# Kernel tuning notes

Measured on AMD Instinct MI355X. Metric: run time of the kernel, lower is better.

## Reference

```python
import jax, jax.numpy as jnp
import numpy as np

N, E, D, H, L = 50000, 800000, 64, 4, 2
DH = D // H


def layer_norm(h, g, b, eps=1e-5):
    mu = h.mean(-1, keepdims=True)
    var = ((h - mu) ** 2).mean(-1, keepdims=True)
    return (h - mu) / jnp.sqrt(var + eps) * g + b


def setup_inputs() -> dict:
    key = jax.random.key(0)
    ks = jax.random.split(key, 16)
    s = 1.0 / np.sqrt(D)
    inp = {
        "x": jax.random.normal(ks[0], (N, D), jnp.float32),
        "edge_attr": jax.random.normal(ks[1], (E, D), jnp.float32),
        "edge_index": jax.random.randint(ks[2], (2, E), 0, N, jnp.int64),
        "WQ": jax.random.normal(ks[3], (L, D, D), jnp.float32) * s,
        "WK": jax.random.normal(ks[4], (L, D, D), jnp.float32) * s,
        "WE": jax.random.normal(ks[5], (L, D, D), jnp.float32) * s,
        "WV": jax.random.normal(ks[6], (L, D, D), jnp.float32) * s,
        "WO": jax.random.normal(ks[7], (L, D, D), jnp.float32) * s,
        "bO": jnp.zeros((L, D), jnp.float32),
        "ln1_g": jnp.ones((L, D), jnp.float32),
        "ln1_b": jnp.zeros((L, D), jnp.float32),
        "W1": jax.random.normal(ks[8], (L, D, 2 * D), jnp.float32) * s,
        "b1": jnp.zeros((L, 2 * D), jnp.float32),
        "W2": jax.random.normal(ks[9], (L, 2 * D, D), jnp.float32) * (1.0 / np.sqrt(2 * D)),
        "b2": jnp.zeros((L, D), jnp.float32),
        "ln2_g": jnp.ones((L, D), jnp.float32),
        "ln2_b": jnp.zeros((L, D), jnp.float32),
    }
    return inp


def exphormer_layer(h, edge_attr, src, dst, p):
    (wq, wk, we, wv, wo, bo, g1, be1, w1, b1, w2, b2, g2, be2) = p
    n = h.shape[0]
    Qh = (h @ wq).reshape(n, H, DH)
    Kh = (h @ wk).reshape(n, H, DH)
    Vh = (h @ wv).reshape(n, H, DH)
    Eh = (edge_attr @ we).reshape(-1, H, DH)
    # per-edge score: sum over head_dim of K[src]*Q[dst]*E / sqrt(DH)
    s = jnp.sum(Kh[src] * Qh[dst] * Eh, axis=-1, keepdims=True) / np.sqrt(DH)
    score = jnp.exp(jnp.clip(s, -5.0, 5.0))  # [E, H, 1]
    msg = Vh[src] * score                     # [E, H, DH]
    wV = jax.ops.segment_sum(msg, dst, num_segments=n)    # [N, H, DH]
    Z = jax.ops.segment_sum(score, dst, num_segments=n)   # [N, H, 1]
    h_attn = (wV / (Z + 1e-6)).reshape(n, D)
    h1 = layer_norm(h + (h_attn @ wo + bo), g1, be1)
    ffn = jax.nn.relu(h1 @ w1 + b1) @ w2 + b2
    return layer_norm(h1 + ffn, g2, be2)


def reference(x, edge_attr, edge_index, WQ, WK, WE, WV, WO, bO, ln1_g, ln1_b,
              W1, b1, W2, b2, ln2_g, ln2_b):
    src = edge_index[0]
    dst = edge_index[1]
    h = x
    for l in range(L):
        p = (WQ[l], WK[l], WE[l], WV[l], WO[l], bO[l], ln1_g[l], ln1_b[l],
             W1[l], b1[l], W2[l], b2[l], ln2_g[l], ln2_b[l])
        h = exphormer_layer(h, edge_attr, src, dst, p)
    return h
```

## Files before the change

kernel.cpp:

```cpp
#include <hip/hip_runtime.h>

#define NN 50000
#define NE 800000
#define D  64
#define NL 2
#define NB 196

typedef __bf16 bf16x8 __attribute__((ext_vector_type(8)));
typedef float  floatx4 __attribute__((ext_vector_type(4)));

static __device__ __forceinline__ float bf2f(unsigned short u) {
    return __uint_as_float(((unsigned)u) << 16);
}
static __device__ __forceinline__ unsigned short f2bf(float x) {
    unsigned u = __float_as_uint(x);
    u += 0x7fff + ((u >> 16) & 1);
    return (unsigned short)(u >> 16);
}


__global__ void k_deg(const int* __restrict__ ei, int* __restrict__ deg) {
    int e = blockIdx.x * 256 + threadIdx.x;
    if (e < NE) atomicAdd(&deg[ei[NE + e]], 1);
}

__global__ __launch_bounds__(256) void k_scan1(const int* __restrict__ deg,
                                               int* __restrict__ psum) {
    __shared__ int red[4];
    int i = blockIdx.x * 256 + threadIdx.x;
    int v = (i < NN) ? deg[i] : 0;
#pragma unroll
    for (int m = 1; m < 64; m <<= 1) v += __shfl_xor(v, m, 64);
    if ((threadIdx.x & 63) == 0) red[threadIdx.x >> 6] = v;
    __syncthreads();
    if (threadIdx.x == 0) psum[blockIdx.x] = red[0] + red[1] + red[2] + red[3];
}

__global__ void k_scan2(int* __restrict__ psum) {
    __shared__ int buf[256];
    int t = threadIdx.x;
    int v = (t < NB) ? psum[t] : 0;
    buf[t] = v;
    __syncthreads();
    for (int o = 1; o < 256; o <<= 1) {
        int x = (t >= o) ? buf[t - o] : 0;
        __syncthreads();
        buf[t] += x;
        __syncthreads();
    }
    if (t < NB) psum[t] = buf[t] - v;
}

__global__ __launch_bounds__(256) void k_scan3(const int* __restrict__ deg,
                                               const int* __restrict__ psum,
                                               int* __restrict__ row_off,
                                               int* __restrict__ cursor) {
    __shared__ int buf[256];
    int t = threadIdx.x;
    int i = blockIdx.x * 256 + t;
    int v = (i < NN) ? deg[i] : 0;
    buf[t] = v;
    __syncthreads();
    for (int o = 1; o < 256; o <<= 1) {
        int x = (t >= o) ? buf[t - o] : 0;
        __syncthreads();
        buf[t] += x;
        __syncthreads();
    }
    if (i < NN) {
        int inc = buf[t] + psum[blockIdx.x];
        row_off[i + 1] = inc;
        cursor[i] = inc - v;
        if (i == 0) row_off[0] = 0;
    }
}

__global__ void k_scatter(const int* __restrict__ ei, int* __restrict__ cursor,
                          int* __restrict__ csr_src, int* __restrict__ eperm) {
    int e = blockIdx.x * 256 + threadIdx.x;
    if (e < NE) {
        int dst = ei[NE + e];
        int pos = atomicAdd(&cursor[dst], 1);
        csr_src[pos] = ei[e];
        eperm[e] = pos;
    }
}

__global__ __launch_bounds__(256) void k_prep(
        const float* __restrict__ WQ, const float* __restrict__ WK,
        const float* __restrict__ WV, const float* __restrict__ WE,
        const float* __restrict__ WO, const float* __restrict__ W1,
        const float* __restrict__ W2,
        unsigned short* __restrict__ wqT, unsigned short* __restrict__ wkT,
        unsigned short* __restrict__ wvT, unsigned short* __restrict__ weT,
        unsigned short* __restrict__ woT, unsigned short* __restrict__ w1T,
        unsigned short* __restrict__ w2T) {
    int idx = blockIdx.x * 256 + threadIdx.x;
    if (idx >= 2 * 36864) return;
    int l = idx / 36864;
    int r = idx % 36864;
    if (r < 20480) {
        int which = r >> 12, rr = r & 4095;
        int m = rr >> 6, k = rr & 63;
        const float* src = (which == 0 ? WQ : which == 1 ? WK : which == 2 ? WV :
                            which == 3 ? WE : WO);
        unsigned short* dst = (which == 0 ? wqT : which == 1 ? wkT : which == 2 ? wvT :
                               which == 3 ? weT : woT);
        dst[l * 4096 + rr] = f2bf(src[l * 4096 + k * 64 + m]);
    } else if (r < 28672) {
        int r2 = r - 20480;
        int m = r2 >> 6, k = r2 & 63;
        w1T[l * 8192 + r2] = f2bf(W1[l * 8192 + k * 128 + m]);
    } else {
        int r3 = r - 28672;
        int m = r3 >> 7, k = r3 & 127;
        w2T[l * 8192 + r3] = f2bf(W2[l * 8192 + k * 64 + m]);
    }
}


__global__ __launch_bounds__(256) void k_qkv_mfma(const float* __restrict__ h,
        const unsigned short* __restrict__ wqT, const unsigned short* __restrict__ wkT,
        const unsigned short* __restrict__ wvT,
        float* __restrict__ Qh, unsigned short* __restrict__ Kb,
        unsigned short* __restrict__ Vb) {
    __shared__ unsigned short st[4][16 * 72];
    const int lane = threadIdx.x & 63;
    const int w    = threadIdx.x >> 6;
    const int ml   = lane & 15;
    const int quad = lane >> 4;

    bf16x8 aq[2][4], ak[2][4], av[2][4];
#pragma unroll
    for (int kt = 0; kt < 2; kt++)
#pragma unroll
        for (int mt = 0; mt < 4; mt++) {
            int o = (mt*16 + ml)*64 + kt*32 + quad*8;
            aq[kt][mt] = *(const bf16x8*)&wqT[o];
            ak[kt][mt] = *(const bf16x8*)&wkT[o];
            av[kt][mt] = *(const bf16x8*)&wvT[o];
        }

    const int wave = blockIdx.x * 4 + w;
    const int nw   = gridDim.x * 4;
    for (int tile = wave; tile < NN / 16; tile += nw) {
        const int e0 = tile * 16;
        const float4* ar = (const float4*)(h + (size_t)(e0 + ml) * D);
        bf16x8 b[2];
#pragma unroll
        for (int kt = 0; kt < 2; kt++) {
            float4 f0 = ar[kt*8 + quad*2 + 0];
            float4 f1 = ar[kt*8 + quad*2 + 1];
            b[kt][0] = (__bf16)f0.x; b[kt][1] = (__bf16)f0.y;
            b[kt][2] = (__bf16)f0.z; b[kt][3] = (__bf16)f0.w;
            b[kt][4] = (__bf16)f1.x; b[kt][5] = (__bf16)f1.y;
            b[kt][6] = (__bf16)f1.z; b[kt][7] = (__bf16)f1.w;
        }
        floatx4 accq[4] = {}, acck[4] = {}, accv[4] = {};
#pragma unroll
        for (int kt = 0; kt < 2; kt++)
#pragma unroll
            for (int mt = 0; mt < 4; mt++) {
                accq[mt] = __builtin_amdgcn_mfma_f32_16x16x32_bf16(aq[kt][mt], b[kt], accq[mt], 0, 0, 0);
                acck[mt] = __builtin_amdgcn_mfma_f32_16x16x32_bf16(ak[kt][mt], b[kt], acck[mt], 0, 0, 0);
                accv[mt] = __builtin_amdgcn_mfma_f32_16x16x32_bf16(av[kt][mt], b[kt], accv[mt], 0, 0, 0);
            }
#pragma unroll
        for (int mt = 0; mt < 4; mt++)
            *(float4*)(Qh + (size_t)(e0 + ml) * D + mt*16 + quad*4) =
                make_float4(accq[mt][0], accq[mt][1], accq[mt][2], accq[mt][3]);
        const int el = lane >> 2, c = lane & 3;
#pragma unroll
        for (int mt = 0; mt < 4; mt++)
            *(ushort4*)&st[w][ml*72 + mt*16 + quad*4] =
                make_ushort4(f2bf(acck[mt][0]), f2bf(acck[mt][1]),
                             f2bf(acck[mt][2]), f2bf(acck[mt][3]));
        {
            uint4 r0 = *(const uint4*)&st[w][el*72 + c*16 + 0];
            uint4 r1 = *(const uint4*)&st[w][el*72 + c*16 + 8];
            uint4* gp = (uint4*)(Kb + (size_t)(e0 + el) * D + c*16);
            gp[0] = r0; gp[1] = r1;
        }
#pragma unroll
        for (int mt = 0; mt < 4; mt++)
            *(ushort4*)&st[w][ml*72 + mt*16 + quad*4] =
                make_ushort4(f2bf(accv[mt][0]), f2bf(accv[mt][1]),
                             f2bf(accv[mt][2]), f2bf(accv[mt][3]));
        {
            uint4 r0 = *(const uint4*)&st[w][el*72 + c*16 + 0];
            uint4 r1 = *(const uint4*)&st[w][el*72 + c*16 + 8];
            uint4* gp = (uint4*)(Vb + (size_t)(e0 + el) * D + c*16);
            gp[0] = r0; gp[1] = r1;
        }
    }
}

__global__ __launch_bounds__(256) void k_eh_mfma(const float* __restrict__ ea,
        const unsigned short* __restrict__ weT, const int* __restrict__ eperm,
        unsigned short* __restrict__ Eh) {
    __shared__ unsigned short st[4][16 * 72];
    const int lane = threadIdx.x & 63;
    const int w    = threadIdx.x >> 6;
    const int ml   = lane & 15;
    const int quad = lane >> 4;

    bf16x8 afr[2][2][4];
#pragma unroll
    for (int l = 0; l < 2; l++)
#pragma unroll
        for (int kt = 0; kt < 2; kt++)
#pragma unroll
            for (int mt = 0; mt < 4; mt++)
                afr[l][kt][mt] = *(const bf16x8*)&weT[l*4096 + (mt*16 + ml)*64 + kt*32 + quad*8];

    const int wave = blockIdx.x * 4 + w;
    const int nw   = gridDim.x * 4;
    const int el = lane >> 2, c = lane & 3;
    for (int tile = wave; tile < NE / 16; tile += nw) {
        const int e0 = tile * 16;
        const float4* ar = (const float4*)(ea + (size_t)(e0 + ml) * D);
        bf16x8 b[2];
#pragma unroll
        for (int kt = 0; kt < 2; kt++) {
            float4 f0 = ar[kt*8 + quad*2 + 0];
            float4 f1 = ar[kt*8 + quad*2 + 1];
            b[kt][0] = (__bf16)f0.x; b[kt][1] = (__bf16)f0.y;
            b[kt][2] = (__bf16)f0.z; b[kt][3] = (__bf16)f0.w;
            b[kt][4] = (__bf16)f1.x; b[kt][5] = (__bf16)f1.y;
            b[kt][6] = (__bf16)f1.z; b[kt][7] = (__bf16)f1.w;
        }
        int pos = eperm[e0 + el];
#pragma unroll
        for (int l = 0; l < 2; l++) {
            floatx4 acc[4] = {};
#pragma unroll
            for (int kt = 0; kt < 2; kt++)
#pragma unroll
                for (int mt = 0; mt < 4; mt++)
                    acc[mt] = __builtin_amdgcn_mfma_f32_16x16x32_bf16(afr[l][kt][mt], b[kt], acc[mt], 0, 0, 0);
#pragma unroll
            for (int mt = 0; mt < 4; mt++)
                *(ushort4*)&st[w][ml*72 + mt*16 + quad*4] =
                    make_ushort4(f2bf(acc[mt][0]), f2bf(acc[mt][1]),
                                 f2bf(acc[mt][2]), f2bf(acc[mt][3]));
            uint4 r0 = *(const uint4*)&st[w][el*72 + c*16 + 0];
            uint4 r1 = *(const uint4*)&st[w][el*72 + c*16 + 8];
            uint4* gp = (uint4*)(Eh + (size_t)l * NE * D + (size_t)pos * D + c*16);
            gp[0] = r0;
            gp[1] = r1;
        }
    }
}

__global__ __launch_bounds__(256) void k_agg(const float* __restrict__ Qh,
        const unsigned short* __restrict__ Kb, const unsigned short* __restrict__ Vb,
        const unsigned short* __restrict__ Eh,
        const int* __restrict__ row_off, const int* __restrict__ csr_src,
        float* __restrict__ h_attn) {
    const int node = blockIdx.x * 4 + (threadIdx.x >> 6);
    if (node >= NN) return;
    const int lane  = threadIdx.x & 63;
    const int eslot = lane >> 4;
    const int ml    = lane & 15;
    const int beg = row_off[node], end = row_off[node + 1];
    const float4 q = ((const float4*)(Qh + (size_t)node * D))[ml];
    float4 acc = make_float4(0.f, 0.f, 0.f, 0.f);
    float z = 0.f;

    for (int cbeg = beg; cbeg < end; cbeg += 64) {
        const int cnt = min(64, end - cbeg);
        int myidx = cbeg + lane;
        int mysrc = (myidx < end) ? csr_src[myidx] : 0;

        for (int base = 0; base < cnt; base += 16) {
            int  jj[4];
            int  s[4];
            bool act[4];
#pragma unroll
            for (int u = 0; u < 4; u++) {
                int j = base + eslot + 4 * u;
                act[u] = j < cnt;
                jj[u]  = act[u] ? j : 0;
                s[u]   = __shfl(mysrc, jj[u], 64);
            }
            ushort4 kb[4], eb[4], vb[4];
#pragma unroll
            for (int u = 0; u < 4; u++) {
                kb[u] = *(const ushort4*)(Kb + (size_t)s[u] * D + ml * 4);
                eb[u] = *(const ushort4*)(Eh + (size_t)(cbeg + jj[u]) * D + ml * 4);
                vb[u] = *(const ushort4*)(Vb + (size_t)s[u] * D + ml * 4);
            }
#pragma unroll
            for (int u = 0; u < 4; u++) {
                float part = bf2f(kb[u].x) * q.x * bf2f(eb[u].x)
                           + bf2f(kb[u].y) * q.y * bf2f(eb[u].y)
                           + bf2f(kb[u].z) * q.z * bf2f(eb[u].z)
                           + bf2f(kb[u].w) * q.w * bf2f(eb[u].w);
                part += __shfl_xor(part, 1, 64);
                part += __shfl_xor(part, 2, 64);
                float sc = act[u] ? __expf(fminf(5.f, fmaxf(-5.f, part * 0.25f))) : 0.f;
                acc.x += sc * bf2f(vb[u].x);
                acc.y += sc * bf2f(vb[u].y);
                acc.z += sc * bf2f(vb[u].z);
                acc.w += sc * bf2f(vb[u].w);
                z += sc;
            }
        }
    }
#pragma unroll
    for (int m = 16; m <= 32; m <<= 1) {
        acc.x += __shfl_xor(acc.x, m, 64);
        acc.y += __shfl_xor(acc.y, m, 64);
        acc.z += __shfl_xor(acc.z, m, 64);
        acc.w += __shfl_xor(acc.w, m, 64);
        z     += __shfl_xor(z, m, 64);
    }
    if (eslot == 0) {
        float inv = 1.f / (z + 1e-6f);
        ((float4*)(h_attn + (size_t)node * D))[ml] =
            make_float4(acc.x * inv, acc.y * inv, acc.z * inv, acc.w * inv);
    }
}

__global__ __launch_bounds__(512) void k_post_mfma(const float* __restrict__ h_in,
        const float* __restrict__ h_attn,
        const unsigned short* __restrict__ woT_g,
        const unsigned short* __restrict__ w1T_g,
        const unsigned short* __restrict__ w2T_g,
        const float* __restrict__ bo,
        const float* __restrict__ g1, const float* __restrict__ be1,
        const float* __restrict__ b1, const float* __restrict__ b2,
        const float* __restrict__ g2, const float* __restrict__ be2,
        float* __restrict__ h_out) {
    __shared__ unsigned short woT_s[64 * 72];
    __shared__ unsigned short w1T_s[128 * 72];
    __shared__ unsigned short w2T_s[64 * 136];
    __shared__ unsigned short stg[8][16 * 136];

    const int t = threadIdx.x;
    {
        const uint4* s0 = (const uint4*)woT_g;
        { int i = t; if (i < 512) { int row = i >> 3, c = i & 7;
              *(uint4*)&woT_s[row*72 + c*8] = s0[i]; } }
        const uint4* s1 = (const uint4*)w1T_g;
        for (int i = t; i < 1024; i += 512) {
            int row = i >> 3, c = i & 7;
            *(uint4*)&w1T_s[row*72 + c*8] = s1[i];
        }
        const uint4* s2 = (const uint4*)w2T_g;
        for (int i = t; i < 1024; i += 512) {
            int row = i >> 4, c = i & 15;
            *(uint4*)&w2T_s[row*136 + c*8] = s2[i];
        }
    }
    __syncthreads();

    const int w = t >> 6, lane = t & 63;
    const int ml = lane & 15, quad = lane >> 4;
    const int tile = blockIdx.x * 8 + w;
    if (tile >= NN / 16) return;
    const int e0 = tile * 16;
    unsigned short* st = stg[w];

    const float4* ap = (const float4*)(h_attn + (size_t)(e0 + ml) * D);
    floatx4 acc1[4] = {};
#pragma unroll
    for (int kt = 0; kt < 2; kt++) {
        float4 f0 = ap[kt*8 + quad*2 + 0];
        float4 f1 = ap[kt*8 + quad*2 + 1];
        bf16x8 b;
        b[0] = (__bf16)f0.x; b[1] = (__bf16)f0.y; b[2] = (__bf16)f0.z; b[3] = (__bf16)f0.w;
        b[4] = (__bf16)f1.x; b[5] = (__bf16)f1.y; b[6] = (__bf16)f1.z; b[7] = (__bf16)f1.w;
#pragma unroll
        for (int mt = 0; mt < 4; mt++) {
            bf16x8 a = *(const bf16x8*)&woT_s[(mt*16 + ml)*72 + kt*32 + quad*8];
            acc1[mt] = __builtin_amdgcn_mfma_f32_16x16x32_bf16(a, b, acc1[mt], 0, 0, 0);
        }
    }
    const float4* hp  = (const float4*)(h_in + (size_t)(e0 + ml) * D);
    const float4* bo4 = (const float4*)bo;
    floatx4 tt[4];
#pragma unroll
    for (int mt = 0; mt < 4; mt++) {
        float4 hh = hp[mt*4 + quad];
        float4 bb = bo4[mt*4 + quad];
        tt[mt][0] = acc1[mt][0] + hh.x + bb.x;
        tt[mt][1] = acc1[mt][1] + hh.y + bb.y;
        tt[mt][2] = acc1[mt][2] + hh.z + bb.z;
        tt[mt][3] = acc1[mt][3] + hh.w + bb.w;
    }
    float s = 0.f;
#pragma unroll
    for (int mt = 0; mt < 4; mt++) s += tt[mt][0] + tt[mt][1] + tt[mt][2] + tt[mt][3];
    s += __shfl_xor(s, 16, 64); s += __shfl_xor(s, 32, 64);
    float mu = s * (1.f / 64.f);
    float v = 0.f;
#pragma unroll
    for (int mt = 0; mt < 4; mt++)
#pragma unroll
        for (int r = 0; r < 4; r++) { float c = tt[mt][r] - mu; v += c * c; }
    v += __shfl_xor(v, 16, 64); v += __shfl_xor(v, 32, 64);
    float rstd = rsqrtf(v * (1.f / 64.f) + 1e-5f);
    const float4* g1v  = (const float4*)g1;
    const float4* be1v = (const float4*)be1;
    floatx4 h1[4];
#pragma unroll
    for (int mt = 0; mt < 4; mt++) {
        float4 gg = g1v[mt*4 + quad];
        float4 bb = be1v[mt*4 + quad];
        h1[mt][0] = (tt[mt][0] - mu) * rstd * gg.x + bb.x;
        h1[mt][1] = (tt[mt][1] - mu) * rstd * gg.y + bb.y;
        h1[mt][2] = (tt[mt][2] - mu) * rstd * gg.z + bb.z;
        h1[mt][3] = (tt[mt][3] - mu) * rstd * gg.w + bb.w;
        *(ushort4*)&st[ml*136 + mt*16 + quad*4] =
            make_ushort4(f2bf(h1[mt][0]), f2bf(h1[mt][1]), f2bf(h1[mt][2]), f2bf(h1[mt][3]));
    }

    bf16x8 bh[2];
#pragma unroll
    for (int kt = 0; kt < 2; kt++)
        bh[kt] = *(const bf16x8*)&st[ml*136 + kt*32 + quad*8];
    floatx4 acc2[8] = {};
#pragma unroll
    for (int kt = 0; kt < 2; kt++)
#pragma unroll
        for (int mt = 0; mt < 8; mt++) {
            bf16x8 a = *(const bf16x8*)&w1T_s[(mt*16 + ml)*72 + kt*32 + quad*8];
            acc2[mt] = __builtin_amdgcn_mfma_f32_16x16x32_bf16(a, bh[kt], acc2[mt], 0, 0, 0);
        }
    const float4* b1v = (const float4*)b1;
#pragma unroll
    for (int mt = 0; mt < 8; mt++) {
        float4 bb = b1v[mt*4 + quad];
        float y0 = fmaxf(acc2[mt][0] + bb.x, 0.f);
        float y1 = fmaxf(acc2[mt][1] + bb.y, 0.f);
        float y2 = fmaxf(acc2[mt][2] + bb.z, 0.f);
        float y3 = fmaxf(acc2[mt][3] + bb.w, 0.f);
        *(ushort4*)&st[ml*136 + mt*16 + quad*4] =
            make_ushort4(f2bf(y0), f2bf(y1), f2bf(y2), f2bf(y3));
    }

    floatx4 acc3[4] = {};
#pragma unroll
    for (int kt = 0; kt < 4; kt++) {
        bf16x8 b = *(const bf16x8*)&st[ml*136 + kt*32 + quad*8];
#pragma unroll
        for (int mt = 0; mt < 4; mt++) {
            bf16x8 a = *(const bf16x8*)&w2T_s[(mt*16 + ml)*136 + kt*32 + quad*8];
            acc3[mt] = __builtin_amdgcn_mfma_f32_16x16x32_bf16(a, b, acc3[mt], 0, 0, 0);
        }
    }
    const float4* b2v = (const float4*)b2;
#pragma unroll
    for (int mt = 0; mt < 4; mt++) {
        float4 bb = b2v[mt*4 + quad];
        tt[mt][0] = acc3[mt][0] + bb.x + h1[mt][0];
        tt[mt][1] = acc3[mt][1] + bb.y + h1[mt][1];
        tt[mt][2] = acc3[mt][2] + bb.z + h1[mt][2];
        tt[mt][3] = acc3[mt][3] + bb.w + h1[mt][3];
    }
    s = 0.f;
#pragma unroll
    for (int mt = 0; mt < 4; mt++) s += tt[mt][0] + tt[mt][1] + tt[mt][2] + tt[mt][3];
    s += __shfl_xor(s, 16, 64); s += __shfl_xor(s, 32, 64);
    mu = s * (1.f / 64.f);
    v = 0.f;
#pragma unroll
    for (int mt = 0; mt < 4; mt++)
#pragma unroll
        for (int r = 0; r < 4; r++) { float c = tt[mt][r] - mu; v += c * c; }
    v += __shfl_xor(v, 16, 64); v += __shfl_xor(v, 32, 64);
    rstd = rsqrtf(v * (1.f / 64.f) + 1e-5f);
    const float4* g2v  = (const float4*)g2;
    const float4* be2v = (const float4*)be2;
    float4* outp = (float4*)(h_out + (size_t)(e0 + ml) * D);
#pragma unroll
    for (int mt = 0; mt < 4; mt++) {
        float4 gg = g2v[mt*4 + quad];
        float4 bb = be2v[mt*4 + quad];
        float4 o;
        o.x = (tt[mt][0] - mu) * rstd * gg.x + bb.x;
        o.y = (tt[mt][1] - mu) * rstd * gg.y + bb.y;
        o.z = (tt[mt][2] - mu) * rstd * gg.z + bb.z;
        o.w = (tt[mt][3] - mu) * rstd * gg.w + bb.w;
        outp[mt*4 + quad] = o;
    }
}


extern "C" void kernel_launch(void* const* d_in, const int* in_sizes, int n_in,
                              void* d_out, int out_size, void* d_ws, size_t ws_size,
                              hipStream_t stream) {
    const float* x   = (const float*)d_in[0];
    const float* ea  = (const float*)d_in[1];
    const int*   ei  = (const int*)d_in[2];
    const float* WQ  = (const float*)d_in[3];
    const float* WK  = (const float*)d_in[4];
    const float* WE  = (const float*)d_in[5];
    const float* WV  = (const float*)d_in[6];
    const float* WO  = (const float*)d_in[7];
    const float* bO  = (const float*)d_in[8];
    const float* g1  = (const float*)d_in[9];
    const float* be1 = (const float*)d_in[10];
    const float* W1  = (const float*)d_in[11];
    const float* b1  = (const float*)d_in[12];
    const float* W2  = (const float*)d_in[13];
    const float* b2  = (const float*)d_in[14];
    const float* g2  = (const float*)d_in[15];
    const float* be2 = (const float*)d_in[16];
    float* out = (float*)d_out;

    char* wsb = (char*)d_ws;
    size_t off = 0;
    auto alloc = [&](size_t bytes) {
        void* p = wsb + off;
        off += (bytes + 255) & ~(size_t)255;
        return p;
    };
    float* Qh            = (float*)alloc((size_t)NN * D * 4);
    unsigned short* Kb   = (unsigned short*)alloc((size_t)NN * D * 2);
    unsigned short* Vb   = (unsigned short*)alloc((size_t)NN * D * 2);
    float* hbuf          = (float*)alloc((size_t)NN * D * 4);
    float* hattn         = (float*)alloc((size_t)NN * D * 4);
    unsigned short* Eh   = (unsigned short*)alloc((size_t)NL * NE * D * 2);
    int* row_off         = (int*)alloc((size_t)(NN + 1) * 4);
    int* cursor          = (int*)alloc((size_t)NN * 4);
    int* deg             = (int*)alloc((size_t)NN * 4);
    int* psum            = (int*)alloc((size_t)256 * 4);
    int* csr_src         = (int*)alloc((size_t)NE * 4);
    int* eperm           = (int*)alloc((size_t)NE * 4);
    unsigned short* wqT  = (unsigned short*)alloc((size_t)2 * 4096 * 2);
    unsigned short* wkT  = (unsigned short*)alloc((size_t)2 * 4096 * 2);
    unsigned short* wvT  = (unsigned short*)alloc((size_t)2 * 4096 * 2);
    unsigned short* weT  = (unsigned short*)alloc((size_t)2 * 4096 * 2);
    unsigned short* woT  = (unsigned short*)alloc((size_t)2 * 4096 * 2);
    unsigned short* w1T  = (unsigned short*)alloc((size_t)2 * 8192 * 2);
    unsigned short* w2T  = (unsigned short*)alloc((size_t)2 * 8192 * 2);

    hipMemsetAsync(deg, 0, (size_t)NN * 4, stream);
    k_deg<<<(NE + 255) / 256, 256, 0, stream>>>(ei, deg);
    k_scan1<<<NB, 256, 0, stream>>>(deg, psum);
    k_scan2<<<1, 256, 0, stream>>>(psum);
    k_scan3<<<NB, 256, 0, stream>>>(deg, psum, row_off, cursor);
    k_scatter<<<(NE + 255) / 256, 256, 0, stream>>>(ei, cursor, csr_src, eperm);
    k_prep<<<(2 * 36864 + 255) / 256, 256, 0, stream>>>(WQ, WK, WV, WE, WO, W1, W2,
            wqT, wkT, wvT, weT, woT, w1T, w2T);
    k_eh_mfma<<<1024, 256, 0, stream>>>(ea, weT, eperm, Eh);

    for (int l = 0; l < NL; l++) {
        const float* hcur = (l == 0) ? x : hbuf;
        float* hnxt = (l == NL - 1) ? out : hbuf;
        k_qkv_mfma<<<782, 256, 0, stream>>>(hcur, wqT + l * 4096, wkT + l * 4096,
                                            wvT + l * 4096, Qh, Kb, Vb);
        k_agg<<<(NN + 3) / 4, 256, 0, stream>>>(Qh, Kb, Vb, Eh + (size_t)l * NE * D,
                                                row_off, csr_src, hattn);
        k_post_mfma<<<(NN / 16 + 7) / 8, 512, 0, stream>>>(hcur, hattn,
                woT + l * 4096, w1T + l * 8192, w2T + l * 8192,
                bO + l * 64, g1 + l * 64, be1 + l * 64,
                b1 + l * 128, b2 + l * 64,
                g2 + l * 64, be2 + l * 64, hnxt);
    }
}
```

Measured before the change: 611.3 us.

## Fuse layer-0 edge scores into Eh projection, split score computation from aggregation

The layer-0 edge-attribute projection now computes the per-edge attention scores directly from MFMA accumulators, so the layer-0 Eh is never written to memory. Layer-1 scores are computed by a separate edge-parallel kernel in CSR order. Aggregation then reads only V and the precomputed scores instead of gathering K, Q and Eh per edge. This removes one large bf16 Eh buffer and the redundant per-head K/Eh gathers in the aggregation, but adds a score buffer round-trip, extra random Q/K gathers in edge order, and a csr_dst array.

```diff
diff --git a/kernel.cpp b/kernel.cpp
--- a/kernel.cpp
+++ b/kernel.cpp
@@ -76,12 +76,14 @@
 }
 
 __global__ void k_scatter(const int* __restrict__ ei, int* __restrict__ cursor,
-                          int* __restrict__ csr_src, int* __restrict__ eperm) {
+                          int* __restrict__ csr_src, int* __restrict__ csr_dst,
+                          int* __restrict__ eperm) {
     int e = blockIdx.x * 256 + threadIdx.x;
     if (e < NE) {
         int dst = ei[NE + e];
         int pos = atomicAdd(&cursor[dst], 1);
         csr_src[pos] = ei[e];
+        csr_dst[pos] = dst;
         eperm[e] = pos;
     }
 }
@@ -195,9 +197,11 @@
     }
 }
 
-__global__ __launch_bounds__(256) void k_eh_mfma(const float* __restrict__ ea,
+__global__ __launch_bounds__(256) void k_eh_score(const float* __restrict__ ea,
         const unsigned short* __restrict__ weT, const int* __restrict__ eperm,
-        unsigned short* __restrict__ Eh) {
+        const int* __restrict__ ei, const float* __restrict__ Qh,
+        const unsigned short* __restrict__ Kb,
+        float* __restrict__ scb, unsigned short* __restrict__ Eh1) {
     __shared__ unsigned short st[4][16 * 72];
     const int lane = threadIdx.x & 63;
     const int w    = threadIdx.x >> 6;
@@ -229,15 +233,43 @@
             b[kt][4] = (__bf16)f1.x; b[kt][5] = (__bf16)f1.y;
             b[kt][6] = (__bf16)f1.z; b[kt][7] = (__bf16)f1.w;
         }
-        int pos = eperm[e0 + el];
-#pragma unroll
-        for (int l = 0; l < 2; l++) {
+        const int eid  = e0 + ml;
+        const int srcn = ei[eid];
+        const int dstn = ei[NE + eid];
+        const int posm = eperm[eid];
+        const int pose = eperm[e0 + el];
+
+        {
             floatx4 acc[4] = {};
 #pragma unroll
             for (int kt = 0; kt < 2; kt++)
 #pragma unroll
                 for (int mt = 0; mt < 4; mt++)
-                    acc[mt] = __builtin_amdgcn_mfma_f32_16x16x32_bf16(afr[l][kt][mt], b[kt], acc[mt], 0, 0, 0);
+                    acc[mt] = __builtin_amdgcn_mfma_f32_16x16x32_bf16(afr[0][kt][mt], b[kt], acc[mt], 0, 0, 0);
+            float scq[4];
+#pragma unroll
+            for (int mt = 0; mt < 4; mt++) {
+                float4 q4 = *(const float4*)(Qh + (size_t)dstn * D + mt*16 + quad*4);
+                ushort4 k4 = *(const ushort4*)(Kb + (size_t)srcn * D + mt*16 + quad*4);
+                float p = acc[mt][0] * q4.x * bf2f(k4.x)
+                        + acc[mt][1] * q4.y * bf2f(k4.y)
+                        + acc[mt][2] * q4.z * bf2f(k4.z)
+                        + acc[mt][3] * q4.w * bf2f(k4.w);
+                p += __shfl_xor(p, 16, 64);
+                p += __shfl_xor(p, 32, 64);
+                scq[mt] = __expf(fminf(5.f, fmaxf(-5.f, p * 0.25f)));
+            }
+            if (quad == 0)
+                *(float4*)(scb + (size_t)posm * 4) =
+                    make_float4(scq[0], scq[1], scq[2], scq[3]);
+        }
+        {
+            floatx4 acc[4] = {};
+#pragma unroll
+            for (int kt = 0; kt < 2; kt++)
+#pragma unroll
+                for (int mt = 0; mt < 4; mt++)
+                    acc[mt] = __builtin_amdgcn_mfma_f32_16x16x32_bf16(afr[1][kt][mt], b[kt], acc[mt], 0, 0, 0);
 #pragma unroll
             for (int mt = 0; mt < 4; mt++)
                 *(ushort4*)&st[w][ml*72 + mt*16 + quad*4] =
@@ -245,16 +277,56 @@
                                  f2bf(acc[mt][2]), f2bf(acc[mt][3]));
             uint4 r0 = *(const uint4*)&st[w][el*72 + c*16 + 0];
             uint4 r1 = *(const uint4*)&st[w][el*72 + c*16 + 8];
-            uint4* gp = (uint4*)(Eh + (size_t)l * NE * D + (size_t)pos * D + c*16);
+            uint4* gp = (uint4*)(Eh1 + (size_t)pose * D + c*16);
             gp[0] = r0;
             gp[1] = r1;
         }
     }
 }
 
-__global__ __launch_bounds__(256) void k_agg(const float* __restrict__ Qh,
-        const unsigned short* __restrict__ Kb, const unsigned short* __restrict__ Vb,
-        const unsigned short* __restrict__ Eh,
+__global__ __launch_bounds__(256) void k_score1(
+        const unsigned short* __restrict__ Eh1,
+        const float* __restrict__ Qh, const unsigned short* __restrict__ Kb,
+        const int* __restrict__ csr_src, const int* __restrict__ csr_dst,
+        float* __restrict__ scb) {
+    const int lane = threadIdx.x & 63;
+    const int w    = threadIdx.x >> 6;
+    const int ml   = lane & 15;
+    const int quad = lane >> 4;
+    const int wave = blockIdx.x * 4 + w;
+    const int nw   = gridDim.x * 4;
+    for (int tile = wave; tile < NE / 16; tile += nw) {
+        const int p = tile * 16 + ml;
+        const int src = csr_src[p];
+        const int dst = csr_dst[p];
+        bf16x8 e0v = *(const bf16x8*)(Eh1 + (size_t)p * D + quad*16);
+        bf16x8 e1v = *(const bf16x8*)(Eh1 + (size_t)p * D + quad*16 + 8);
+        bf16x8 k0v = *(const bf16x8*)(Kb + (size_t)src * D + quad*16);
+        bf16x8 k1v = *(const bf16x8*)(Kb + (size_t)src * D + quad*16 + 8);
+        const float4* qp = (const float4*)(Qh + (size_t)dst * D + quad*16);
+        float4 q0 = qp[0], q1 = qp[1], q2 = qp[2], q3 = qp[3];
+        float s = (float)e0v[0] * q0.x * (float)k0v[0]
+                + (float)e0v[1] * q0.y * (float)k0v[1]
+                + (float)e0v[2] * q0.z * (float)k0v[2]
+                + (float)e0v[3] * q0.w * (float)k0v[3]
+                + (float)e0v[4] * q1.x * (float)k0v[4]
+                + (float)e0v[5] * q1.y * (float)k0v[5]
+                + (float)e0v[6] * q1.z * (float)k0v[6]
+                + (float)e0v[7] * q1.w * (float)k0v[7]
+                + (float)e1v[0] * q2.x * (float)k1v[0]
+                + (float)e1v[1] * q2.y * (float)k1v[1]
+                + (float)e1v[2] * q2.z * (float)k1v[2]
+                + (float)e1v[3] * q2.w * (float)k1v[3]
+                + (float)e1v[4] * q3.x * (float)k1v[4]
+                + (float)e1v[5] * q3.y * (float)k1v[5]
+                + (float)e1v[6] * q3.z * (float)k1v[6]
+                + (float)e1v[7] * q3.w * (float)k1v[7];
+        scb[(size_t)p * 4 + quad] = __expf(fminf(5.f, fmaxf(-5.f, s * 0.25f)));
+    }
+}
+
+__global__ __launch_bounds__(256) void k_agg(
+        const unsigned short* __restrict__ Vb, const float* __restrict__ scb,
         const int* __restrict__ row_off, const int* __restrict__ csr_src,
         float* __restrict__ h_attn) {
     const int node = blockIdx.x * 4 + (threadIdx.x >> 6);
@@ -262,8 +334,8 @@
     const int lane  = threadIdx.x & 63;
     const int eslot = lane >> 4;
     const int ml    = lane & 15;
+    const int hsel  = ml >> 2;
     const int beg = row_off[node], end = row_off[node + 1];
-    const float4 q = ((const float4*)(Qh + (size_t)node * D))[ml];
     float4 acc = make_float4(0.f, 0.f, 0.f, 0.f);
     float z = 0.f;
 
@@ -283,22 +355,16 @@
                 jj[u]  = act[u] ? j : 0;
                 s[u]   = __shfl(mysrc, jj[u], 64);
             }
-            ushort4 kb[4], eb[4], vb[4];
+            ushort4 vb[4];
+            float   sv[4];
 #pragma unroll
             for (int u = 0; u < 4; u++) {
-                kb[u] = *(const ushort4*)(Kb + (size_t)s[u] * D + ml * 4);
-                eb[u] = *(const ushort4*)(Eh + (size_t)(cbeg + jj[u]) * D + ml * 4);
                 vb[u] = *(const ushort4*)(Vb + (size_t)s[u] * D + ml * 4);
+                sv[u] = scb[(size_t)(cbeg + jj[u]) * 4 + hsel];
             }
 #pragma unroll
             for (int u = 0; u < 4; u++) {
-                float part = bf2f(kb[u].x) * q.x * bf2f(eb[u].x)
-                           + bf2f(kb[u].y) * q.y * bf2f(eb[u].y)
-                           + bf2f(kb[u].z) * q.z * bf2f(eb[u].z)
-                           + bf2f(kb[u].w) * q.w * bf2f(eb[u].w);
-                part += __shfl_xor(part, 1, 64);
-                part += __shfl_xor(part, 2, 64);
-                float sc = act[u] ? __expf(fminf(5.f, fmaxf(-5.f, part * 0.25f))) : 0.f;
+                float sc = act[u] ? sv[u] : 0.f;
                 acc.x += sc * bf2f(vb[u].x);
                 acc.y += sc * bf2f(vb[u].y);
                 acc.z += sc * bf2f(vb[u].z);
@@ -522,12 +588,14 @@
     unsigned short* Vb   = (unsigned short*)alloc((size_t)NN * D * 2);
     float* hbuf          = (float*)alloc((size_t)NN * D * 4);
     float* hattn         = (float*)alloc((size_t)NN * D * 4);
-    unsigned short* Eh   = (unsigned short*)alloc((size_t)NL * NE * D * 2);
+    unsigned short* Eh1  = (unsigned short*)alloc((size_t)NE * D * 2);
+    float* scb           = (float*)alloc((size_t)NE * 4 * 4);
     int* row_off         = (int*)alloc((size_t)(NN + 1) * 4);
     int* cursor          = (int*)alloc((size_t)NN * 4);
     int* deg             = (int*)alloc((size_t)NN * 4);
     int* psum            = (int*)alloc((size_t)256 * 4);
     int* csr_src         = (int*)alloc((size_t)NE * 4);
+    int* csr_dst         = (int*)alloc((size_t)NE * 4);
     int* eperm           = (int*)alloc((size_t)NE * 4);
     unsigned short* wqT  = (unsigned short*)alloc((size_t)2 * 4096 * 2);
     unsigned short* wkT  = (unsigned short*)alloc((size_t)2 * 4096 * 2);
@@ -542,22 +610,23 @@
     k_scan1<<<NB, 256, 0, stream>>>(deg, psum);
     k_scan2<<<1, 256, 0, stream>>>(psum);
     k_scan3<<<NB, 256, 0, stream>>>(deg, psum, row_off, cursor);
-    k_scatter<<<(NE + 255) / 256, 256, 0, stream>>>(ei, cursor, csr_src, eperm);
+    k_scatter<<<(NE + 255) / 256, 256, 0, stream>>>(ei, cursor, csr_src, csr_dst, eperm);
     k_prep<<<(2 * 36864 + 255) / 256, 256, 0, stream>>>(WQ, WK, WV, WE, WO, W1, W2,
             wqT, wkT, wvT, weT, woT, w1T, w2T);
-    k_eh_mfma<<<1024, 256, 0, stream>>>(ea, weT, eperm, Eh);
-
-    for (int l = 0; l < NL; l++) {
-        const float* hcur = (l == 0) ? x : hbuf;
-        float* hnxt = (l == NL - 1) ? out : hbuf;
-        k_qkv_mfma<<<782, 256, 0, stream>>>(hcur, wqT + l * 4096, wkT + l * 4096,
-                                            wvT + l * 4096, Qh, Kb, Vb);
-        k_agg<<<(NN + 3) / 4, 256, 0, stream>>>(Qh, Kb, Vb, Eh + (size_t)l * NE * D,
-                                                row_off, csr_src, hattn);
-        k_post_mfma<<<(NN / 16 + 7) / 8, 512, 0, stream>>>(hcur, hattn,
-                woT + l * 4096, w1T + l * 8192, w2T + l * 8192,
-                bO + l * 64, g1 + l * 64, be1 + l * 64,
-                b1 + l * 128, b2 + l * 64,
-                g2 + l * 64, be2 + l * 64, hnxt);
-    }
-}
+
+    k_qkv_mfma<<<782, 256, 0, stream>>>(x, wqT, wkT, wvT, Qh, Kb, Vb);
+    k_eh_score<<<1536, 256, 0, stream>>>(ea, weT, eperm, ei, Qh, Kb, scb, Eh1);
+
+    k_agg<<<(NN + 3) / 4, 256, 0, stream>>>(Vb, scb, row_off, csr_src, hattn);
+    k_post_mfma<<<(NN / 16 + 7) / 8, 512, 0, stream>>>(x, hattn,
+            woT, w1T, w2T, bO, g1, be1, b1, b2, g2, be2, hbuf);
+
+    k_qkv_mfma<<<782, 256, 0, stream>>>(hbuf, wqT + 4096, wkT + 4096,
+                                        wvT + 4096, Qh, Kb, Vb);
+    k_score1<<<1536, 256, 0, stream>>>(Eh1, Qh, Kb, csr_src, csr_dst, scb);
+    k_agg<<<(NN + 3) / 4, 256, 0, stream>>>(Vb, scb, row_off, csr_src, hattn);
+    k_post_mfma<<<(NN / 16 + 7) / 8, 512, 0, stream>>>(hbuf, hattn,
+            woT + 4096, w1T + 8192, w2T + 8192,
+            bO + 64, g1 + 64, be1 + 64, b1 + 128, b2 + 64,
+            g2 + 64, be2 + 64, out);
+}
```

After: 619.6 us. No clear change (+1.4%).
